# Optimization experiments

Measured on AMD Instinct MI355X. Metric: run time of the kernel, lower is better.

Reference implementation:

```python
import math
import jax, jax.numpy as jnp
import numpy as np

N, B, C, H, K = 1024, 8, 512, 8, 5  # seq len, batch, d_model, heads, near_kth
NEG = -1.0e9


def setup_inputs() -> dict:
    key = jax.random.key(0)
    ks = jax.random.split(key, 10)
    s = 0.02
    return {
        "query": jax.random.normal(ks[0], (N, B, C), jnp.float32),
        "key_t": jax.random.normal(ks[1], (N, B, C), jnp.float32),
        "value": jax.random.normal(ks[2], (N, B, C), jnp.float32),
        "src_position": jax.random.normal(ks[3], (N, B, 3), jnp.float32),
        "tgt_position": jax.random.normal(ks[4], (N, B, 3), jnp.float32),
        # nn.MultiheadAttention params (in_proj split into q/k/v, plus out_proj)
        "Wq": jax.random.normal(ks[5], (C, C), jnp.float32) * s,
        "Wk": jax.random.normal(ks[6], (C, C), jnp.float32) * s,
        "Wv": jax.random.normal(ks[7], (C, C), jnp.float32) * s,
        "bq": jnp.zeros((C,), jnp.float32),
        "bk": jnp.zeros((C,), jnp.float32),
        "bv": jnp.zeros((C,), jnp.float32),
        "Wo": jax.random.normal(ks[8], (C, C), jnp.float32) * s,
        "bo": jnp.zeros((C,), jnp.float32),
    }


def reference(query, key_t, value, src_position, tgt_position,
              Wq, Wk, Wv, bq, bk, bv, Wo, bo):
    # --- 'nearby' positional mask ---------------------------------------
    # dist[b, tgt, src] = ||src_position[src,b] - tgt_position[tgt,b]||^2
    diff = src_position[None, :, :, :] - tgt_position[:, None, :, :]  # (Nt,Ns,B,3)
    dist = jnp.sum(diff * diff, axis=-1).transpose(2, 0, 1)           # (B,Nt,Ns)
    # torch: topk(dist, k=5, dim=1, largest=False) -> 5 nearest TARGETS per source
    _, idx = jax.lax.top_k(-dist.transpose(0, 2, 1), K)               # (B,Ns,K) tgt idx
    mask = jnp.full((B, N, N), NEG, jnp.float32)
    b_i = jnp.arange(B)[:, None, None]
    s_i = jnp.arange(N)[None, :, None]
    mask = mask.at[b_i, idx, s_i].set(0.0)                            # (B,Nt,Ns)

    # --- multihead attention (eval mode, dropout=0) ----------------------
    hd = C // H
    scale = 1.0 / math.sqrt(hd)
    q = ((query @ Wq.T + bq) * scale).reshape(N, B, H, hd)
    k = (key_t @ Wk.T + bk).reshape(N, B, H, hd)
    v = (value @ Wv.T + bv).reshape(N, B, H, hd)
    scores = jnp.einsum('tbhd,sbhd->bhts', q, k) + mask[:, None]      # (B,H,Nt,Ns)
    attn = jax.nn.softmax(scores, axis=-1)
    ctx = jnp.einsum('bhts,sbhd->tbhd', attn, v).reshape(N, B, C)
    out = ctx @ Wo.T + bo                                             # (N,B,C)
    attn_avg = attn.mean(axis=1)                                      # (B,Nt,Ns)
    return out, attn_avg
```

## Files before the change

kernel.cpp:

```cpp
#include <hip/hip_runtime.h>
#include <cstdint>
#include <cstddef>

#define NSEQ 1024
#define BATCH 8
#define CMODEL 512
#define NHEAD 8
#define HDIM 64
#define CAP 64
#define FLTMAX 3.402823466e+38f

typedef short bf16x8 __attribute__((ext_vector_type(8)));
typedef float f32x4 __attribute__((ext_vector_type(4)));
typedef unsigned short ushort8v __attribute__((ext_vector_type(8)));
typedef unsigned short ushort2v __attribute__((ext_vector_type(2)));

__device__ inline unsigned short f2bf(float f) {
    unsigned int u = __builtin_bit_cast(unsigned int, f);
    u += 0x7fffu + ((u >> 16) & 1u);
    return (unsigned short)(u >> 16);
}

__global__ __launch_bounds__(256) void convert_w(const float* __restrict__ w0,
                                                 const float* __restrict__ w1,
                                                 const float* __restrict__ w2,
                                                 const float* __restrict__ w3,
                                                 unsigned short* __restrict__ o0,
                                                 unsigned short* __restrict__ o1,
                                                 unsigned short* __restrict__ o2,
                                                 unsigned short* __restrict__ o3,
                                                 unsigned int* __restrict__ zp) {
    if (blockIdx.x >= 512) {
        const int zi = (blockIdx.x - 512) * 256 + threadIdx.x;
        zp[zi] = 0u;
        return;
    }
    const int idx = blockIdx.x * 256 + threadIdx.x;
    const int rgn = idx >> 15;
    const int c   = idx & 32767;
    const float* src = rgn == 0 ? w0 : rgn == 1 ? w1 : rgn == 2 ? w2 : w3;
    unsigned short* dst = rgn == 0 ? o0 : rgn == 1 ? o1 : rgn == 2 ? o2 : o3;
    const float4 v0 = *(const float4*)(src + (size_t)c * 8);
    const float4 v1 = *(const float4*)(src + (size_t)c * 8 + 4);
    ushort8v u;
    u[0] = f2bf(v0.x); u[1] = f2bf(v0.y); u[2] = f2bf(v0.z); u[3] = f2bf(v0.w);
    u[4] = f2bf(v1.x); u[5] = f2bf(v1.y); u[6] = f2bf(v1.z); u[7] = f2bf(v1.w);
    *(ushort8v*)(dst + (size_t)c * 8) = u;
}

__global__ __launch_bounds__(256) void topk_scatter(const float* __restrict__ srcp,
                                                    const float* __restrict__ tgtp,
                                                    int* __restrict__ row_cnt,
                                                    int* __restrict__ row_list) {
    const int w = threadIdx.x >> 6, lane = threadIdx.x & 63;
    const int wg = blockIdx.x * 4 + w;
    const int s = wg & 1023, b = wg >> 10;

    const float sx = srcp[((size_t)s * BATCH + b) * 3 + 0];
    const float sy = srcp[((size_t)s * BATCH + b) * 3 + 1];
    const float sz = srcp[((size_t)s * BATCH + b) * 3 + 2];

    float dv[16];
    #pragma unroll
    for (int i = 0; i < 16; ++i) {
        const int t = i * 64 + lane;
        const float dx = tgtp[((size_t)t * BATCH + b) * 3 + 0] - sx;
        const float dy = tgtp[((size_t)t * BATCH + b) * 3 + 1] - sy;
        const float dz = tgtp[((size_t)t * BATCH + b) * 3 + 2] - sz;
        dv[i] = dx * dx + dy * dy + dz * dz;
    }

    #pragma unroll
    for (int k = 0; k < 5; ++k) {
        float bvv = FLTMAX;
        int   bii = 0x7fffffff;
        #pragma unroll
        for (int i = 0; i < 16; ++i) {
            if (dv[i] < bvv) { bvv = dv[i]; bii = i * 64 + lane; }
        }
        #pragma unroll
        for (int off = 1; off < 64; off <<= 1) {
            const float ov = __shfl_xor(bvv, off);
            const int   oi = __shfl_xor(bii, off);
            if (ov < bvv || (ov == bvv && oi < bii)) { bvv = ov; bii = oi; }
        }
        if (lane == (bii & 63)) {
            #pragma unroll
            for (int i = 0; i < 16; ++i)
                if (bii == i * 64 + lane) dv[i] = FLTMAX;
        }
        if (lane == 0) {
            const int pos = atomicAdd(&row_cnt[b * NSEQ + bii], 1);
            if (pos < CAP) row_list[((size_t)b * NSEQ + bii) * CAP + pos] = s;
        }
    }
}

template<int AMODE, int OMODE>
__device__ inline void gemm_body(const void* __restrict__ Ap,
                                 const unsigned short* __restrict__ Wbf,
                                 const float* __restrict__ bias,
                                 float* __restrict__ out,
                                 float scale) {
    __shared__ __align__(16) char smem[12288];
    const int tid = threadIdx.x;
    const int l = tid & 63, w = tid >> 6;
    const int m0 = blockIdx.x * 128, n0 = blockIdx.y * 64;
    const int wr = (w >> 1) * 64, wc = (w & 1) * 32;
    const int lr = l & 15, g = l >> 4;

    f32x4 acc[4][2] = {};

    const int rowB = w * 16 + (l >> 2);
    const int gkB  = (l & 3) ^ ((rowB >> 1) & 3);
    const unsigned short* bsrc = Wbf + (size_t)(n0 + rowB) * CMODEL + gkB * 8;
    char* bdst = smem + 8192 + w * 1024;

    const float* asrc0 = nullptr; const float* asrc1 = nullptr;
    char* adst0 = nullptr; char* adst1 = nullptr;
    const unsigned short* asrcW0 = nullptr; const unsigned short* asrcW1 = nullptr;
    char* adstW0 = nullptr; char* adstW1 = nullptr;
    if constexpr (AMODE == 0) {
        const int rowA = tid >> 2;
        const int slA  = tid & 3;
        const int gkA  = slA ^ ((rowA >> 1) & 3);
        asrc0 = (const float*)Ap + (size_t)(m0 + rowA) * CMODEL + gkA * 8;
        asrc1 = asrc0 + (size_t)64 * CMODEL;
        adst0 = smem + rowA * 64 + slA * 16;
        adst1 = adst0 + 64 * 64;
    } else {
        const unsigned short* Abf = (const unsigned short*)Ap;
        const int rA0 = w * 16 + (l >> 2);
        const int gk0 = (l & 3) ^ ((rA0 >> 1) & 3);
        asrcW0 = Abf + (size_t)(m0 + rA0) * CMODEL + gk0 * 8;
        asrcW1 = asrcW0 + (size_t)64 * CMODEL;
        adstW0 = smem + w * 1024;
        adstW1 = adstW0 + 4096;
    }

    for (int k0 = 0; k0 < CMODEL; k0 += 32) {
        float4 a00, a01, a10, a11;
        if constexpr (AMODE == 0) {
            a00 = *(const float4*)(asrc0 + k0);
            a01 = *(const float4*)(asrc0 + k0 + 4);
            a10 = *(const float4*)(asrc1 + k0);
            a11 = *(const float4*)(asrc1 + k0 + 4);
        }
        __syncthreads();

        __builtin_amdgcn_global_load_lds(
            (const __attribute__((address_space(1))) void*)(bsrc + k0),
            (__attribute__((address_space(3))) void*)bdst, 16, 0, 0);

        if constexpr (AMODE == 0) {
            ushort8v u0, u1;
            u0[0] = f2bf(a00.x); u0[1] = f2bf(a00.y); u0[2] = f2bf(a00.z); u0[3] = f2bf(a00.w);
            u0[4] = f2bf(a01.x); u0[5] = f2bf(a01.y); u0[6] = f2bf(a01.z); u0[7] = f2bf(a01.w);
            u1[0] = f2bf(a10.x); u1[1] = f2bf(a10.y); u1[2] = f2bf(a10.z); u1[3] = f2bf(a10.w);
            u1[4] = f2bf(a11.x); u1[5] = f2bf(a11.y); u1[6] = f2bf(a11.z); u1[7] = f2bf(a11.w);
            *(ushort8v*)adst0 = u0;
            *(ushort8v*)adst1 = u1;
        } else {
            __builtin_amdgcn_global_load_lds(
                (const __attribute__((address_space(1))) void*)(asrcW0 + k0),
                (__attribute__((address_space(3))) void*)adstW0, 16, 0, 0);
            __builtin_amdgcn_global_load_lds(
                (const __attribute__((address_space(1))) void*)(asrcW1 + k0),
                (__attribute__((address_space(3))) void*)adstW1, 16, 0, 0);
        }
        __syncthreads();

        bf16x8 af[4], bfr[2];
        #pragma unroll
        for (int i = 0; i < 4; ++i) {
            const int ra = wr + i * 16 + lr;
            af[i] = *(const bf16x8*)(smem + ra * 64 + ((g ^ ((ra >> 1) & 3)) << 4));
        }
        #pragma unroll
        for (int j = 0; j < 2; ++j) {
            const int rb = wc + j * 16 + lr;
            bfr[j] = *(const bf16x8*)(smem + 8192 + rb * 64 + ((g ^ ((rb >> 1) & 3)) << 4));
        }
        #pragma unroll
        for (int i = 0; i < 4; ++i)
            #pragma unroll
            for (int j = 0; j < 2; ++j)
                acc[i][j] = __builtin_amdgcn_mfma_f32_16x16x32_bf16(af[i], bfr[j], acc[i][j], 0, 0, 0);
    }

    #pragma unroll
    for (int i = 0; i < 4; ++i) {
        #pragma unroll
        for (int j = 0; j < 2; ++j) {
            const int col = n0 + wc + j * 16 + lr;
            const float bcol = bias[col];
            #pragma unroll
            for (int r = 0; r < 4; ++r) {
                const int row = m0 + wr + i * 16 + g * 4 + r;
                const float val = (acc[i][j][r] + bcol) * scale;
                if constexpr (OMODE == 0) {
                    const int t = row >> 3, bb = row & 7;
                    out[((size_t)(bb * NSEQ + t)) * CMODEL + col] = val;
                } else {
                    out[(size_t)row * CMODEL + col] = val;
                }
            }
        }
    }
}

__global__ __launch_bounds__(256, 2) void gemm_proj(const float* __restrict__ Aq,
                                                    const float* __restrict__ Ak,
                                                    const float* __restrict__ Av,
                                                    const unsigned short* __restrict__ Wq,
                                                    const unsigned short* __restrict__ Wk,
                                                    const unsigned short* __restrict__ Wv,
                                                    const float* __restrict__ bq,
                                                    const float* __restrict__ bk,
                                                    const float* __restrict__ bv,
                                                    float* __restrict__ oq,
                                                    float* __restrict__ ok,
                                                    float* __restrict__ ov) {
    const int z = blockIdx.z;
    const float* A = z == 0 ? Aq : z == 1 ? Ak : Av;
    const unsigned short* W = z == 0 ? Wq : z == 1 ? Wk : Wv;
    const float* bi = z == 0 ? bq : z == 1 ? bk : bv;
    float* o = z == 0 ? oq : z == 1 ? ok : ov;
    const float sc = z == 0 ? 0.125f : 1.0f;
    gemm_body<0, 0>(A, W, bi, o, sc);
}

__global__ __launch_bounds__(256, 2) void gemm_out(const unsigned short* __restrict__ Abf,
                                                   const unsigned short* __restrict__ Wbf,
                                                   const float* __restrict__ bias,
                                                   float* __restrict__ out) {
    gemm_body<1, 1>(Abf, Wbf, bias, out, 1.0f);
}

__global__ __launch_bounds__(512) void v_mean_k(const float* __restrict__ v,
                                                float* __restrict__ vm) {
    const int b = blockIdx.x;
    const int chunk = blockIdx.y;
    const int c = threadIdx.x;
    float s = 0.f;
    const int t0 = chunk * 64;
    for (int t = 0; t < 64; ++t)
        s += v[((size_t)b * NSEQ + t0 + t) * CMODEL + c];
    atomicAdd(&vm[b * CMODEL + c], s * (1.f / (float)NSEQ));
}

__global__ __launch_bounds__(256) void sparse_attn(const float* __restrict__ q_ws,
                                                   const float* __restrict__ k_ws,
                                                   const float* __restrict__ v_ws,
                                                   const int* __restrict__ row_cnt,
                                                   const int* __restrict__ row_list,
                                                   const float* __restrict__ vm,
                                                   unsigned short* __restrict__ ctx,
                                                   float* __restrict__ attn_out) {
    const int t = blockIdx.x;
    const int b = blockIdx.y;
    const int tid = threadIdx.x;

    int cnt = row_cnt[b * NSEQ + t];
    if (cnt > CAP) cnt = CAP;

    float* arow = attn_out + ((size_t)b * NSEQ + t) * NSEQ;

    if (cnt == 0) {
        const float u = 1.f / (float)NSEQ;
        const float4 uv = {u, u, u, u};
        ((float4*)arow)[tid] = uv;
        for (int c = tid; c < CMODEL; c += 256)
            ctx[((size_t)t * BATCH + b) * CMODEL + c] = f2bf(vm[b * CMODEL + c]);
        return;
    }

    {
        const float4 zv = {0.f, 0.f, 0.f, 0.f};
        ((float4*)arow)[tid] = zv;
    }

    __shared__ float qs[CMODEL];
    __shared__ float esc[CAP][8];
    __shared__ float denom[8];
    __shared__ int   slist[CAP];

    if (tid < 8) denom[tid] = 0.f;
    if (tid < cnt) slist[tid] = row_list[((size_t)b * NSEQ + t) * CAP + tid];
    {
        const float2 qv = *(const float2*)(q_ws + ((size_t)b * NSEQ + t) * CMODEL + tid * 2);
        qs[tid * 2] = qv.x; qs[tid * 2 + 1] = qv.y;
    }
    __syncthreads();

    const int wid = tid >> 6, lane = tid & 63;
    for (int i = wid; i < cnt; i += 4) {
        const int s = slist[i];
        const float* krow = k_ws + ((size_t)b * NSEQ + s) * CMODEL + lane * 8;
        const float* qrow = qs + lane * 8;
        float part = 0.f;
        #pragma unroll
        for (int j = 0; j < 8; ++j) part += qrow[j] * krow[j];
        part += __shfl_xor(part, 1);
        part += __shfl_xor(part, 2);
        part += __shfl_xor(part, 4);
        if ((lane & 7) == 0) {
            const int h = lane >> 3;
            const float e = __expf(part);
            esc[i][h] = e;
            atomicAdd(&denom[h], e);
        }
    }
    __syncthreads();

    for (int x = tid; x < cnt * 8; x += 256)
        esc[x >> 3][x & 7] /= denom[x & 7];
    __syncthreads();

    for (int i = tid; i < cnt; i += 256) {
        float pm = 0.f;
        #pragma unroll
        for (int h = 0; h < 8; ++h) pm += esc[i][h];
        arow[slist[i]] = pm * 0.125f;
    }

    const int c0 = tid * 2;
    const int h0 = c0 >> 6;
    float acc0 = 0.f, acc1 = 0.f;
    for (int i = 0; i < cnt; ++i) {
        const int s = slist[i];
        const float p = esc[i][h0];
        const float2 vv = *(const float2*)(v_ws + ((size_t)b * NSEQ + s) * CMODEL + c0);
        acc0 += p * vv.x; acc1 += p * vv.y;
    }
    unsigned short* crow = ctx + ((size_t)t * BATCH + b) * CMODEL;
    ushort2v cv; cv[0] = f2bf(acc0); cv[1] = f2bf(acc1);
    *(ushort2v*)(crow + c0) = cv;
}

extern "C" void kernel_launch(void* const* d_in, const int* in_sizes, int n_in,
                              void* d_out, int out_size, void* d_ws, size_t ws_size,
                              hipStream_t stream) {
    (void)in_sizes; (void)n_in; (void)out_size; (void)ws_size;

    const float* query = (const float*)d_in[0];
    const float* key_t = (const float*)d_in[1];
    const float* value = (const float*)d_in[2];
    const float* srcp  = (const float*)d_in[3];
    const float* tgtp  = (const float*)d_in[4];
    const float* Wq    = (const float*)d_in[5];
    const float* Wk    = (const float*)d_in[6];
    const float* Wv    = (const float*)d_in[7];
    const float* bq    = (const float*)d_in[8];
    const float* bk    = (const float*)d_in[9];
    const float* bv    = (const float*)d_in[10];
    const float* Wo    = (const float*)d_in[11];
    const float* bo    = (const float*)d_in[12];

    float* out      = (float*)d_out;
    float* attn_out = out + (size_t)NSEQ * BATCH * CMODEL;

    const size_t NBC = (size_t)BATCH * NSEQ * CMODEL;
    const size_t WSZ = (size_t)CMODEL * CMODEL;
    float* q_ws = (float*)d_ws;
    float* k_ws = q_ws + NBC;
    float* v_ws = k_ws + NBC;
    unsigned short* ctxbf = (unsigned short*)(v_ws + NBC);
    unsigned short* wqbf  = ctxbf + NBC;
    unsigned short* wkbf  = wqbf + WSZ;
    unsigned short* wvbf  = wkbf + WSZ;
    unsigned short* wobf  = wvbf + WSZ;
    int*   row_cnt  = (int*)(wobf + WSZ);
    float* vm       = (float*)(row_cnt + BATCH * NSEQ);
    int*   row_list = (int*)(vm + BATCH * CMODEL);

    convert_w<<<560, 256, 0, stream>>>(Wq, Wk, Wv, Wo, wqbf, wkbf, wvbf, wobf,
                                       (unsigned int*)row_cnt);

    topk_scatter<<<2048, 256, 0, stream>>>(srcp, tgtp, row_cnt, row_list);

    gemm_proj<<<dim3(64, 8, 3), 256, 0, stream>>>(query, key_t, value,
                                                  wqbf, wkbf, wvbf,
                                                  bq, bk, bv,
                                                  q_ws, k_ws, v_ws);

    v_mean_k<<<dim3(BATCH, 16), 512, 0, stream>>>(v_ws, vm);

    sparse_attn<<<dim3(NSEQ, BATCH), 256, 0, stream>>>(q_ws, k_ws, v_ws, row_cnt,
                                                       row_list, vm, ctxbf, attn_out);

    gemm_out<<<dim3(64, 8), 256, 0, stream>>>(ctxbf, wobf, bo, out);
}
```

Baseline: 101.5 us.

## Double-buffer GEMM LDS tiles and store Q/K/V projections as bf16

```diff
diff --git a/kernel.cpp b/kernel.cpp
--- a/kernel.cpp
+++ b/kernel.cpp
@@ -20,6 +20,13 @@
     u += 0x7fffu + ((u >> 16) & 1u);
     return (unsigned short)(u >> 16);
 }
+__device__ inline float bf2f(unsigned short u) {
+    return __builtin_bit_cast(float, (unsigned int)u << 16);
+}
+
+#define GLDS16(gsrc, ldst) \
+    __builtin_amdgcn_global_load_lds((const __attribute__((address_space(1))) void*)(gsrc), \
+                                     (__attribute__((address_space(3))) void*)(ldst), 16, 0, 0)
 
 __global__ __launch_bounds__(256) void convert_w(const float* __restrict__ w0,
                                                  const float* __restrict__ w1,
@@ -100,9 +107,9 @@
 __device__ inline void gemm_body(const void* __restrict__ Ap,
                                  const unsigned short* __restrict__ Wbf,
                                  const float* __restrict__ bias,
-                                 float* __restrict__ out,
+                                 void* __restrict__ outp,
                                  float scale) {
-    __shared__ __align__(16) char smem[12288];
+    __shared__ __align__(16) char smem[24576];
     const int tid = threadIdx.x;
     const int l = tid & 63, w = tid >> 6;
     const int m0 = blockIdx.x * 128, n0 = blockIdx.y * 64;
@@ -114,78 +121,92 @@
     const int rowB = w * 16 + (l >> 2);
     const int gkB  = (l & 3) ^ ((rowB >> 1) & 3);
     const unsigned short* bsrc = Wbf + (size_t)(n0 + rowB) * CMODEL + gkB * 8;
-    char* bdst = smem + 8192 + w * 1024;
+    const int boff = 8192 + w * 1024;
 
     const float* asrc0 = nullptr; const float* asrc1 = nullptr;
-    char* adst0 = nullptr; char* adst1 = nullptr;
+    int adoff0 = 0, adoff1 = 0;
     const unsigned short* asrcW0 = nullptr; const unsigned short* asrcW1 = nullptr;
-    char* adstW0 = nullptr; char* adstW1 = nullptr;
+    int adWoff0 = 0, adWoff1 = 0;
     if constexpr (AMODE == 0) {
         const int rowA = tid >> 2;
         const int slA  = tid & 3;
         const int gkA  = slA ^ ((rowA >> 1) & 3);
         asrc0 = (const float*)Ap + (size_t)(m0 + rowA) * CMODEL + gkA * 8;
         asrc1 = asrc0 + (size_t)64 * CMODEL;
-        adst0 = smem + rowA * 64 + slA * 16;
-        adst1 = adst0 + 64 * 64;
+        adoff0 = rowA * 64 + slA * 16;
+        adoff1 = adoff0 + 4096;
     } else {
         const unsigned short* Abf = (const unsigned short*)Ap;
         const int rA0 = w * 16 + (l >> 2);
         const int gk0 = (l & 3) ^ ((rA0 >> 1) & 3);
         asrcW0 = Abf + (size_t)(m0 + rA0) * CMODEL + gk0 * 8;
         asrcW1 = asrcW0 + (size_t)64 * CMODEL;
-        adstW0 = smem + w * 1024;
-        adstW1 = adstW0 + 4096;
-    }
-
-    for (int k0 = 0; k0 < CMODEL; k0 += 32) {
-        float4 a00, a01, a10, a11;
-        if constexpr (AMODE == 0) {
-            a00 = *(const float4*)(asrc0 + k0);
-            a01 = *(const float4*)(asrc0 + k0 + 4);
-            a10 = *(const float4*)(asrc1 + k0);
-            a11 = *(const float4*)(asrc1 + k0 + 4);
-        }
-        __syncthreads();
-
-        __builtin_amdgcn_global_load_lds(
-            (const __attribute__((address_space(1))) void*)(bsrc + k0),
-            (__attribute__((address_space(3))) void*)bdst, 16, 0, 0);
-
-        if constexpr (AMODE == 0) {
-            ushort8v u0, u1;
-            u0[0] = f2bf(a00.x); u0[1] = f2bf(a00.y); u0[2] = f2bf(a00.z); u0[3] = f2bf(a00.w);
-            u0[4] = f2bf(a01.x); u0[5] = f2bf(a01.y); u0[6] = f2bf(a01.z); u0[7] = f2bf(a01.w);
-            u1[0] = f2bf(a10.x); u1[1] = f2bf(a10.y); u1[2] = f2bf(a10.z); u1[3] = f2bf(a10.w);
-            u1[4] = f2bf(a11.x); u1[5] = f2bf(a11.y); u1[6] = f2bf(a11.z); u1[7] = f2bf(a11.w);
-            *(ushort8v*)adst0 = u0;
-            *(ushort8v*)adst1 = u1;
-        } else {
-            __builtin_amdgcn_global_load_lds(
-                (const __attribute__((address_space(1))) void*)(asrcW0 + k0),
-                (__attribute__((address_space(3))) void*)adstW0, 16, 0, 0);
-            __builtin_amdgcn_global_load_lds(
-                (const __attribute__((address_space(1))) void*)(asrcW1 + k0),
-                (__attribute__((address_space(3))) void*)adstW1, 16, 0, 0);
-        }
-        __syncthreads();
-
+        adWoff0 = w * 1024;
+        adWoff1 = adWoff0 + 4096;
+    }
+
+    float4 a00, a01, a10, a11;
+
+    auto LOADA = [&](int k0) {
+        a00 = *(const float4*)(asrc0 + k0); a01 = *(const float4*)(asrc0 + k0 + 4);
+        a10 = *(const float4*)(asrc1 + k0); a11 = *(const float4*)(asrc1 + k0 + 4);
+    };
+    auto CVTSTORE = [&](int buf) {
+        ushort8v u0, u1;
+        u0[0] = f2bf(a00.x); u0[1] = f2bf(a00.y); u0[2] = f2bf(a00.z); u0[3] = f2bf(a00.w);
+        u0[4] = f2bf(a01.x); u0[5] = f2bf(a01.y); u0[6] = f2bf(a01.z); u0[7] = f2bf(a01.w);
+        u1[0] = f2bf(a10.x); u1[1] = f2bf(a10.y); u1[2] = f2bf(a10.z); u1[3] = f2bf(a10.w);
+        u1[4] = f2bf(a11.x); u1[5] = f2bf(a11.y); u1[6] = f2bf(a11.z); u1[7] = f2bf(a11.w);
+        char* bb = smem + buf * 12288;
+        *(ushort8v*)(bb + adoff0) = u0;
+        *(ushort8v*)(bb + adoff1) = u1;
+    };
+    auto STAGE = [&](int k0, int buf) {
+        char* bb = smem + buf * 12288;
+        GLDS16(bsrc + k0, bb + boff);
+        if constexpr (AMODE == 1) {
+            GLDS16(asrcW0 + k0, bb + adWoff0);
+            GLDS16(asrcW1 + k0, bb + adWoff1);
+        }
+    };
+
+    if constexpr (AMODE == 0) {
+        LOADA(0);
+        STAGE(0, 0);
+        CVTSTORE(0);
+        LOADA(32);
+    } else {
+        STAGE(0, 0);
+    }
+    __syncthreads();
+
+    for (int t = 0; t < 16; ++t) {
+        const int cur = t & 1;
+        if (t < 15) {
+            STAGE((t + 1) * 32, cur ^ 1);
+            if constexpr (AMODE == 0) {
+                CVTSTORE(cur ^ 1);
+                if (t < 14) LOADA((t + 2) * 32);
+            }
+        }
+        char* base = smem + cur * 12288;
         bf16x8 af[4], bfr[2];
         #pragma unroll
         for (int i = 0; i < 4; ++i) {
             const int ra = wr + i * 16 + lr;
-            af[i] = *(const bf16x8*)(smem + ra * 64 + ((g ^ ((ra >> 1) & 3)) << 4));
+            af[i] = *(const bf16x8*)(base + ra * 64 + ((g ^ ((ra >> 1) & 3)) << 4));
         }
         #pragma unroll
         for (int j = 0; j < 2; ++j) {
             const int rb = wc + j * 16 + lr;
-            bfr[j] = *(const bf16x8*)(smem + 8192 + rb * 64 + ((g ^ ((rb >> 1) & 3)) << 4));
+            bfr[j] = *(const bf16x8*)(base + 8192 + rb * 64 + ((g ^ ((rb >> 1) & 3)) << 4));
         }
         #pragma unroll
         for (int i = 0; i < 4; ++i)
             #pragma unroll
             for (int j = 0; j < 2; ++j)
                 acc[i][j] = __builtin_amdgcn_mfma_f32_16x16x32_bf16(af[i], bfr[j], acc[i][j], 0, 0, 0);
+        __syncthreads();
     }
 
     #pragma unroll
@@ -200,16 +221,16 @@
                 const float val = (acc[i][j][r] + bcol) * scale;
                 if constexpr (OMODE == 0) {
                     const int t = row >> 3, bb = row & 7;
-                    out[((size_t)(bb * NSEQ + t)) * CMODEL + col] = val;
+                    ((unsigned short*)outp)[((size_t)(bb * NSEQ + t)) * CMODEL + col] = f2bf(val);
                 } else {
-                    out[(size_t)row * CMODEL + col] = val;
+                    ((float*)outp)[(size_t)row * CMODEL + col] = val;
                 }
             }
         }
     }
 }
 
-__global__ __launch_bounds__(256, 2) void gemm_proj(const float* __restrict__ Aq,
+__global__ __launch_bounds__(256, 4) void gemm_proj(const float* __restrict__ Aq,
                                                     const float* __restrict__ Ak,
                                                     const float* __restrict__ Av,
                                                     const unsigned short* __restrict__ Wq,
@@ -218,26 +239,26 @@
                                                     const float* __restrict__ bq,
                                                     const float* __restrict__ bk,
                                                     const float* __restrict__ bv,
-                                                    float* __restrict__ oq,
-                                                    float* __restrict__ ok,
-                                                    float* __restrict__ ov) {
+                                                    unsigned short* __restrict__ oq,
+                                                    unsigned short* __restrict__ ok,
+                                                    unsigned short* __restrict__ ov) {
     const int z = blockIdx.z;
     const float* A = z == 0 ? Aq : z == 1 ? Ak : Av;
     const unsigned short* W = z == 0 ? Wq : z == 1 ? Wk : Wv;
     const float* bi = z == 0 ? bq : z == 1 ? bk : bv;
-    float* o = z == 0 ? oq : z == 1 ? ok : ov;
+    unsigned short* o = z == 0 ? oq : z == 1 ? ok : ov;
     const float sc = z == 0 ? 0.125f : 1.0f;
     gemm_body<0, 0>(A, W, bi, o, sc);
 }
 
-__global__ __launch_bounds__(256, 2) void gemm_out(const unsigned short* __restrict__ Abf,
+__global__ __launch_bounds__(256, 4) void gemm_out(const unsigned short* __restrict__ Abf,
                                                    const unsigned short* __restrict__ Wbf,
                                                    const float* __restrict__ bias,
                                                    float* __restrict__ out) {
     gemm_body<1, 1>(Abf, Wbf, bias, out, 1.0f);
 }
 
-__global__ __launch_bounds__(512) void v_mean_k(const float* __restrict__ v,
+__global__ __launch_bounds__(512) void v_mean_k(const unsigned short* __restrict__ v,
                                                 float* __restrict__ vm) {
     const int b = blockIdx.x;
     const int chunk = blockIdx.y;
@@ -245,13 +266,13 @@
     float s = 0.f;
     const int t0 = chunk * 64;
     for (int t = 0; t < 64; ++t)
-        s += v[((size_t)b * NSEQ + t0 + t) * CMODEL + c];
+        s += bf2f(v[((size_t)b * NSEQ + t0 + t) * CMODEL + c]);
     atomicAdd(&vm[b * CMODEL + c], s * (1.f / (float)NSEQ));
 }
 
-__global__ __launch_bounds__(256) void sparse_attn(const float* __restrict__ q_ws,
-                                                   const float* __restrict__ k_ws,
-                                                   const float* __restrict__ v_ws,
+__global__ __launch_bounds__(256) void sparse_attn(const unsigned short* __restrict__ q_ws,
+                                                   const unsigned short* __restrict__ k_ws,
+                                                   const unsigned short* __restrict__ v_ws,
                                                    const int* __restrict__ row_cnt,
                                                    const int* __restrict__ row_list,
                                                    const float* __restrict__ vm,
@@ -288,19 +309,19 @@
     if (tid < 8) denom[tid] = 0.f;
     if (tid < cnt) slist[tid] = row_list[((size_t)b * NSEQ + t) * CAP + tid];
     {
-        const float2 qv = *(const float2*)(q_ws + ((size_t)b * NSEQ + t) * CMODEL + tid * 2);
-        qs[tid * 2] = qv.x; qs[tid * 2 + 1] = qv.y;
+        const ushort2v qv = *(const ushort2v*)(q_ws + ((size_t)b * NSEQ + t) * CMODEL + tid * 2);
+        qs[tid * 2] = bf2f(qv[0]); qs[tid * 2 + 1] = bf2f(qv[1]);
     }
     __syncthreads();
 
     const int wid = tid >> 6, lane = tid & 63;
     for (int i = wid; i < cnt; i += 4) {
         const int s = slist[i];
-        const float* krow = k_ws + ((size_t)b * NSEQ + s) * CMODEL + lane * 8;
+        const ushort8v kv = *(const ushort8v*)(k_ws + ((size_t)b * NSEQ + s) * CMODEL + lane * 8);
         const float* qrow = qs + lane * 8;
         float part = 0.f;
         #pragma unroll
-        for (int j = 0; j < 8; ++j) part += qrow[j] * krow[j];
+        for (int j = 0; j < 8; ++j) part += qrow[j] * bf2f(kv[j]);
         part += __shfl_xor(part, 1);
         part += __shfl_xor(part, 2);
         part += __shfl_xor(part, 4);
@@ -330,8 +351,8 @@
     for (int i = 0; i < cnt; ++i) {
         const int s = slist[i];
         const float p = esc[i][h0];
-        const float2 vv = *(const float2*)(v_ws + ((size_t)b * NSEQ + s) * CMODEL + c0);
-        acc0 += p * vv.x; acc1 += p * vv.y;
+        const ushort2v vv = *(const ushort2v*)(v_ws + ((size_t)b * NSEQ + s) * CMODEL + c0);
+        acc0 += p * bf2f(vv[0]); acc1 += p * bf2f(vv[1]);
     }
     unsigned short* crow = ctx + ((size_t)t * BATCH + b) * CMODEL;
     ushort2v cv; cv[0] = f2bf(acc0); cv[1] = f2bf(acc1);
@@ -362,10 +383,10 @@
 
     const size_t NBC = (size_t)BATCH * NSEQ * CMODEL;
     const size_t WSZ = (size_t)CMODEL * CMODEL;
-    float* q_ws = (float*)d_ws;
-    float* k_ws = q_ws + NBC;
-    float* v_ws = k_ws + NBC;
-    unsigned short* ctxbf = (unsigned short*)(v_ws + NBC);
+    unsigned short* q_ws  = (unsigned short*)d_ws;
+    unsigned short* k_ws  = q_ws + NBC;
+    unsigned short* v_ws  = k_ws + NBC;
+    unsigned short* ctxbf = v_ws + NBC;
     unsigned short* wqbf  = ctxbf + NBC;
     unsigned short* wkbf  = wqbf + WSZ;
     unsigned short* wvbf  = wkbf + WSZ;
```

Result: faster. 94.20 us (-7.2%).
